# Optimization experiments

Hardware: AMD Instinct MI355X
Metric: run time of the kernel (lower is better)

The kernel has to match this reference:

```python
import jax, jax.numpy as jnp
import numpy as np

N = 262144
LOC_ENC_LEN = 60
NUM_WEIGHTS = 8
INDIM = 32
OUTDIM = 32
HIDDEN = 32
NEG_SLOPE = 0.01  # nn.LeakyReLU default


def _linear_init(key, fan_in, fan_out):
    # torch nn.Linear default: U(-1/sqrt(fan_in), 1/sqrt(fan_in))
    kw, kb = jax.random.split(key)
    bound = 1.0 / np.sqrt(fan_in)
    w = jax.random.uniform(kw, (fan_in, fan_out), jnp.float32, -bound, bound)
    b = jax.random.uniform(kb, (fan_out,), jnp.float32, -bound, bound)
    return w, b


def setup_inputs() -> dict:
    key = jax.random.key(0)
    ks = jax.random.split(key, 10)
    rel_loc_feat = jax.random.normal(ks[0], (N, LOC_ENC_LEN), jnp.float32)
    feat = jax.random.normal(ks[1], (N, INDIM), jnp.float32)
    dims = [LOC_ENC_LEN, HIDDEN, HIDDEN, HIDDEN, HIDDEN, HIDDEN, NUM_WEIGHTS]
    params = {}
    for i in range(6):
        w, b = _linear_init(ks[2 + i], dims[i], dims[i + 1])
        params[f'sn_w{i}'] = w
        params[f'sn_b{i}'] = b
    # weights_bank: kaiming_normal on [num_weights, indim*outdim] -> std = sqrt(2/fan_in), fan_in = indim*outdim
    std = np.sqrt(2.0 / (INDIM * OUTDIM))
    params['bank'] = jax.random.normal(ks[9], (NUM_WEIGHTS, INDIM * OUTDIM), jnp.float32) * std
    return {'rel_loc_feat': rel_loc_feat, 'feat': feat, **params}


def _score_net(x, ws, bs):
    # 5 Linear+LeakyReLU blocks, then final Linear (no activation)
    for i in range(5):
        x = x @ ws[i] + bs[i]
        x = jnp.where(x >= 0, x, NEG_SLOPE * x)
    return x @ ws[5] + bs[5]


def reference(rel_loc_feat, feat,
              sn_w0, sn_b0, sn_w1, sn_b1, sn_w2, sn_b2,
              sn_w3, sn_b3, sn_w4, sn_b4, sn_w5, sn_b5, bank):
    ws = [sn_w0, sn_w1, sn_w2, sn_w3, sn_w4, sn_w5]
    bs = [sn_b0, sn_b1, sn_b2, sn_b3, sn_b4, sn_b5]
    logits = _score_net(rel_loc_feat, ws, bs)          # [N, num_weights]
    coeff = jax.nn.softmax(logits, axis=-1)            # [N, num_weights]
    # per-point weight matrix: [N, indim*outdim] -> [N, indim, outdim]
    weights = (coeff @ bank).reshape(coeff.shape[0], INDIM, OUTDIM)
    # per-point matmul: feat[:, None] @ weights -> squeeze
    out = jnp.einsum('ni,nio->no', feat, weights)      # [N, outdim]
    return out
```

## Files before the change

### kernel.cpp

```cpp
#include <hip/hip_runtime.h>
#include <stdint.h>


typedef __attribute__((ext_vector_type(8))) __bf16 bf16x8;
typedef __attribute__((ext_vector_type(4))) float f32x4;

union FragU { uint32_t u[4]; bf16x8 v; uint4 q; };

__device__ __forceinline__ unsigned short f2bf(float f) {
    union { float f; uint32_t i; } v; v.f = f;
    return (unsigned short)((v.i + 0x7FFFu + ((v.i >> 16) & 1u)) >> 16);
}
__device__ __forceinline__ float bf2f(uint32_t u16) {
    union { uint32_t i; float f; } v; v.i = u16 << 16; return v.f;
}
__device__ __forceinline__ uint32_t pk2(float x, float y) {
    return (uint32_t)f2bf(x) | ((uint32_t)f2bf(y) << 16);
}
__device__ __forceinline__ int permK(int k) {
    return 4 * (k >> 3) + (k & 3) + 16 * ((k >> 2) & 1);
}
__device__ __forceinline__ f32x4 MF(bf16x8 a, bf16x8 b, f32x4 c) {
    return __builtin_amdgcn_mfma_f32_16x16x32_bf16(a, b, c, 0, 0, 0);
}


struct WPf { const float* p[13]; };

__global__ void pc_prep(WPf wp, uint32_t* __restrict__ ws) {
    int idx = blockIdx.x * blockDim.x + threadIdx.x;
    if (idx >= 10240) return;
    if (idx < 7424) {
        int layer, t, chunk = 0, lane, d; const float* w; bool perm;
        int r = idx;
        if (r < 1024) { chunk = r >> 9; r &= 511; t = r >> 8; r &= 255; lane = r >> 2; d = r & 3;
                        layer = 0; w = wp.p[0]; perm = false; }
        else if (r < 3072) { r -= 1024; layer = 1 + (r >> 9); r &= 511; t = r >> 8; r &= 255;
                             lane = r >> 2; d = r & 3; w = wp.p[2 * layer]; perm = true; }
        else if (r < 3328) { r -= 3072; layer = 5; t = 0; lane = r >> 2; d = r & 3;
                             w = wp.p[10]; perm = true; }
        else { r -= 3328; int bk = r >> 9; r &= 511; t = r >> 8; r &= 255; lane = r >> 2; d = r & 3;
               layer = -1; w = wp.p[12] + bk * 1024; perm = false; }
        int gq = lane >> 4, m = t * 16 + (lane & 15);
        uint32_t o = 0;
        #pragma unroll
        for (int e = 0; e < 2; ++e) {
            int kf = 8 * gq + 2 * d + e;
            float v = 0.f;
            if (layer == -1) {
                v = w[kf * 32 + m];
            } else {
                int ks = perm ? permK(kf) : (chunk * 32 + kf);
                if (layer == 0)      { if (ks < 60) v = w[ks * 32 + m]; }
                else if (layer == 5) { if (m < 8)   v = w[ks * 8 + m]; }
                else                 v = w[ks * 32 + m];
            }
            o |= ((uint32_t)f2bf(v)) << (16 * e);
        }
        ws[idx] = o;
    } else if (idx < 9984) {
        int r = idx - 7424; int L = r >> 9; r &= 511; int t = r >> 8; r &= 255;
        int lane = r >> 2, rr = r & 3;
        ((float*)ws)[idx] = wp.p[2 * L + 1][t * 16 + 4 * (lane >> 4) + rr];
    } else {
        int r = idx - 9984; int lane = r >> 2, rr = r & 3;
        int m = 4 * (lane >> 4) + rr;
        ((float*)ws)[idx] = (m < 8) ? wp.p[11][m] : 0.f;
    }
}

#define IT 2

__global__ __launch_bounds__(256, 4) void pc_main(
    const float* __restrict__ rel, const float* __restrict__ feat,
    const uint32_t* __restrict__ wsu, float* __restrict__ out)
{
    __shared__ __align__(16) uint32_t W[7424];
    {
        uint4* s4 = (uint4*)W;
        const uint4* g4 = (const uint4*)wsu;
        for (int i = threadIdx.x; i < 1856; i += 256) s4[i] = g4[i];
    }
    __syncthreads();

    const int lane = threadIdx.x & 63;
    const int wv = threadIdx.x >> 6;
    const int g = lane >> 4;
    const int n16 = lane & 15;

    const float* bw = (const float*)wsu;
    f32x4 Bi[5][2], Bi5;
    #pragma unroll
    for (int L = 0; L < 5; ++L)
        #pragma unroll
        for (int t = 0; t < 2; ++t) {
            float4 b = ((const float4*)(bw + 7424 + L * 512 + t * 256))[lane];
            Bi[L][t][0] = b.x; Bi[L][t][1] = b.y; Bi[L][t][2] = b.z; Bi[L][t][3] = b.w;
        }
    {
        float4 b = ((const float4*)(bw + 9984))[lane];
        Bi5[0] = b.x; Bi5[1] = b.y; Bi5[2] = b.z; Bi5[3] = b.w;
    }

    const size_t pt0 = (size_t)(blockIdx.x * 4 + wv) * (16 * IT);

    #define LDF(off) ({ FragU _f; _f.q = ((const uint4*)(W + (off)))[lane]; _f.v; })

    #pragma unroll
    for (int it = 0; it < IT; ++it) {
        const size_t n = pt0 + (size_t)it * 16 + n16;

        const float* rrow = rel + n * 60;
        float4 ra = *(const float4*)(rrow + 8 * g);
        float4 rb = *(const float4*)(rrow + 8 * g + 4);
        float4 rc = *(const float4*)(rrow + 32 + 8 * g);
        float4 rd = make_float4(0.f, 0.f, 0.f, 0.f);
        if (g < 3) rd = *(const float4*)(rrow + 36 + 8 * g);
        const float* frow = feat + n * 32 + 8 * g;
        float4 fa = *(const float4*)frow;
        float4 fb = *(const float4*)(frow + 4);

        FragU b0, b1;
        b0.u[0] = pk2(ra.x, ra.y); b0.u[1] = pk2(ra.z, ra.w);
        b0.u[2] = pk2(rb.x, rb.y); b0.u[3] = pk2(rb.z, rb.w);
        b1.u[0] = pk2(rc.x, rc.y); b1.u[1] = pk2(rc.z, rc.w);
        b1.u[2] = pk2(rd.x, rd.y); b1.u[3] = pk2(rd.z, rd.w);

        f32x4 t0 = Bi[0][0], t1 = Bi[0][1];
        t0 = MF(LDF(0),   b0.v, t0); t1 = MF(LDF(256), b0.v, t1);
        t0 = MF(LDF(512), b1.v, t0); t1 = MF(LDF(768), b1.v, t1);

        #pragma unroll
        for (int L = 0; L < 4; ++L) {
            FragU bx;
            #pragma unroll
            for (int r = 0; r < 4; ++r) {
                t0[r] = fmaxf(t0[r], 0.01f * t0[r]);
                t1[r] = fmaxf(t1[r], 0.01f * t1[r]);
            }
            bx.u[0] = pk2(t0[0], t0[1]); bx.u[1] = pk2(t0[2], t0[3]);
            bx.u[2] = pk2(t1[0], t1[1]); bx.u[3] = pk2(t1[2], t1[3]);
            t0 = MF(LDF(1024 + L * 512),       bx.v, Bi[L + 1][0]);
            t1 = MF(LDF(1024 + L * 512 + 256), bx.v, Bi[L + 1][1]);
        }

        {
            FragU bx;
            #pragma unroll
            for (int r = 0; r < 4; ++r) {
                t0[r] = fmaxf(t0[r], 0.01f * t0[r]);
                t1[r] = fmaxf(t1[r], 0.01f * t1[r]);
            }
            bx.u[0] = pk2(t0[0], t0[1]); bx.u[1] = pk2(t0[2], t0[3]);
            bx.u[2] = pk2(t1[0], t1[1]); bx.u[3] = pk2(t1[2], t1[3]);
            t0 = MF(LDF(3072), bx.v, Bi5);
        }

        float m4 = fmaxf(fmaxf(t0[0], t0[1]), fmaxf(t0[2], t0[3]));
        float m8 = fmaxf(m4, __shfl_xor(m4, 16, 64));
        float e0 = __expf(t0[0] - m8), e1 = __expf(t0[1] - m8);
        float e2 = __expf(t0[2] - m8), e3 = __expf(t0[3] - m8);
        float s4 = e0 + e1 + e2 + e3;
        float s8 = s4 + __shfl_xor(s4, 16, 64);
        float inv = 1.0f / s8;
        uint32_t p01 = pk2(e0 * inv, e1 * inv);
        uint32_t p23 = pk2(e2 * inv, e3 * inv);
        uint32_t q01 = (uint32_t)__builtin_amdgcn_ds_bpermute(n16 * 4, (int)p01);
        uint32_t q23 = (uint32_t)__builtin_amdgcn_ds_bpermute(n16 * 4, (int)p23);
        uint32_t q45 = (uint32_t)__builtin_amdgcn_ds_bpermute((n16 + 16) * 4, (int)p01);
        uint32_t q67 = (uint32_t)__builtin_amdgcn_ds_bpermute((n16 + 16) * 4, (int)p23);
        float cw[8] = { bf2f(q01 & 0xffff), bf2f(q01 >> 16),
                        bf2f(q23 & 0xffff), bf2f(q23 >> 16),
                        bf2f(q45 & 0xffff), bf2f(q45 >> 16),
                        bf2f(q67 & 0xffff), bf2f(q67 >> 16) };

        FragU bf_;
        bf_.u[0] = pk2(fa.x, fa.y); bf_.u[1] = pk2(fa.z, fa.w);
        bf_.u[2] = pk2(fb.x, fb.y); bf_.u[3] = pk2(fb.z, fb.w);

        f32x4 o0 = {0.f, 0.f, 0.f, 0.f}, o1 = {0.f, 0.f, 0.f, 0.f};
        #pragma unroll
        for (int k = 0; k < 8; ++k) {
            f32x4 z = {0.f, 0.f, 0.f, 0.f};
            f32x4 u0 = MF(LDF(3328 + k * 512),       bf_.v, z);
            f32x4 u1 = MF(LDF(3328 + k * 512 + 256), bf_.v, z);
            #pragma unroll
            for (int r = 0; r < 4; ++r) {
                o0[r] += cw[k] * u0[r];
                o1[r] += cw[k] * u1[r];
            }
        }

        float* orow = out + n * 32;
        *(float4*)(orow + 4 * g)      = make_float4(o0[0], o0[1], o0[2], o0[3]);
        *(float4*)(orow + 16 + 4 * g) = make_float4(o1[0], o1[1], o1[2], o1[3]);
    }
    #undef LDF
}

extern "C" void kernel_launch(void* const* d_in, const int* in_sizes, int n_in,
                              void* d_out, int out_size, void* d_ws, size_t ws_size,
                              hipStream_t stream)
{
    const float* rel = (const float*)d_in[0];
    const float* feat = (const float*)d_in[1];
    WPf wp;
    for (int i = 0; i < 13; ++i) wp.p[i] = (const float*)d_in[2 + i];
    uint32_t* ws = (uint32_t*)d_ws;
    float* out = (float*)d_out;

    const int npts = in_sizes[0] / 60;
    const int nblocks = npts / (16 * IT * 4);

    hipLaunchKernelGGL(pc_prep, dim3(40), dim3(256), 0, stream, wp, ws);
    hipLaunchKernelGGL(pc_main, dim3(nblocks), dim3(256), 0, stream, rel, feat, ws, out);
}
```

Before: 163.1 us.

## Hold score-net weight fragments in registers, shrink LDS, cheaper bf16 packing

The score-net A fragments (layers 0-5) now load from global memory into registers once per wave, and only the 8 bank fragments stay in LDS (16KB instead of about 29KB). The per-block LDS fill and the per-iteration LDS reads for the MLP go away. Each wave now handles 4 point tiles (IT 4, unroll 2) with launch bounds lowered to 3 blocks/CU to make room for the extra registers. bf16 packing switches to round-half-up plus v_perm, which saves ALU work but changes rounding slightly (no longer round-to-nearest-even).

```diff
diff --git a/kernel.cpp b/kernel.cpp
--- a/kernel.cpp
+++ b/kernel.cpp
@@ -14,8 +14,9 @@
 __device__ __forceinline__ float bf2f(uint32_t u16) {
     union { uint32_t i; float f; } v; v.i = u16 << 16; return v.f;
 }
-__device__ __forceinline__ uint32_t pk2(float x, float y) {
-    return (uint32_t)f2bf(x) | ((uint32_t)f2bf(y) << 16);
+__device__ __forceinline__ uint32_t pk2f(float x, float y) {
+    union { float f; uint32_t i; } a, b; a.f = x; b.f = y;
+    return __builtin_amdgcn_perm(b.i + 0x8000u, a.i + 0x8000u, 0x07060302u);
 }
 __device__ __forceinline__ int permK(int k) {
     return 4 * (k >> 3) + (k & 3) + 16 * ((k >> 2) & 1);
@@ -69,17 +70,18 @@
     }
 }
 
-#define IT 2
-
-__global__ __launch_bounds__(256, 4) void pc_main(
+#define IT 4
+
+__global__ __launch_bounds__(256, 3) void pc_main(
     const float* __restrict__ rel, const float* __restrict__ feat,
     const uint32_t* __restrict__ wsu, float* __restrict__ out)
 {
-    __shared__ __align__(16) uint32_t W[7424];
+    __shared__ __align__(16) uint32_t WB[4096];
     {
-        uint4* s4 = (uint4*)W;
-        const uint4* g4 = (const uint4*)wsu;
-        for (int i = threadIdx.x; i < 1856; i += 256) s4[i] = g4[i];
+        uint4* s4 = (uint4*)WB;
+        const uint4* g4 = (const uint4*)wsu + 832;
+        #pragma unroll
+        for (int i = 0; i < 4; ++i) s4[threadIdx.x + 256 * i] = g4[threadIdx.x + 256 * i];
     }
     __syncthreads();
 
@@ -88,6 +90,18 @@
     const int g = lane >> 4;
     const int n16 = lane & 15;
 
+    #define LDG(off) ({ FragU _f; _f.q = ((const uint4*)(wsu + (off)))[lane]; _f.v; })
+    const bf16x8 A00 = LDG(0),   A01 = LDG(256);
+    const bf16x8 A10 = LDG(512), A11 = LDG(768);
+    bf16x8 A14[4][2];
+    #pragma unroll
+    for (int L = 0; L < 4; ++L) {
+        A14[L][0] = LDG(1024 + L * 512);
+        A14[L][1] = LDG(1024 + L * 512 + 256);
+    }
+    const bf16x8 A5 = LDG(3072);
+    #undef LDG
+
     const float* bw = (const float*)wsu;
     f32x4 Bi[5][2], Bi5;
     #pragma unroll
@@ -104,9 +118,9 @@
 
     const size_t pt0 = (size_t)(blockIdx.x * 4 + wv) * (16 * IT);
 
-    #define LDF(off) ({ FragU _f; _f.q = ((const uint4*)(W + (off)))[lane]; _f.v; })
-
-    #pragma unroll
+    #define LDS_F(off) ({ FragU _f; _f.q = ((const uint4*)(WB + (off)))[lane]; _f.v; })
+
+    #pragma unroll 2
     for (int it = 0; it < IT; ++it) {
         const size_t n = pt0 + (size_t)it * 16 + n16;
 
@@ -121,14 +135,14 @@
         float4 fb = *(const float4*)(frow + 4);
 
         FragU b0, b1;
-        b0.u[0] = pk2(ra.x, ra.y); b0.u[1] = pk2(ra.z, ra.w);
-        b0.u[2] = pk2(rb.x, rb.y); b0.u[3] = pk2(rb.z, rb.w);
-        b1.u[0] = pk2(rc.x, rc.y); b1.u[1] = pk2(rc.z, rc.w);
-        b1.u[2] = pk2(rd.x, rd.y); b1.u[3] = pk2(rd.z, rd.w);
+        b0.u[0] = pk2f(ra.x, ra.y); b0.u[1] = pk2f(ra.z, ra.w);
+        b0.u[2] = pk2f(rb.x, rb.y); b0.u[3] = pk2f(rb.z, rb.w);
+        b1.u[0] = pk2f(rc.x, rc.y); b1.u[1] = pk2f(rc.z, rc.w);
+        b1.u[2] = pk2f(rd.x, rd.y); b1.u[3] = pk2f(rd.z, rd.w);
 
         f32x4 t0 = Bi[0][0], t1 = Bi[0][1];
-        t0 = MF(LDF(0),   b0.v, t0); t1 = MF(LDF(256), b0.v, t1);
-        t0 = MF(LDF(512), b1.v, t0); t1 = MF(LDF(768), b1.v, t1);
+        t0 = MF(A00, b0.v, t0); t1 = MF(A01, b0.v, t1);
+        t0 = MF(A10, b1.v, t0); t1 = MF(A11, b1.v, t1);
 
         #pragma unroll
         for (int L = 0; L < 4; ++L) {
@@ -138,10 +152,10 @@
                 t0[r] = fmaxf(t0[r], 0.01f * t0[r]);
                 t1[r] = fmaxf(t1[r], 0.01f * t1[r]);
             }
-            bx.u[0] = pk2(t0[0], t0[1]); bx.u[1] = pk2(t0[2], t0[3]);
-            bx.u[2] = pk2(t1[0], t1[1]); bx.u[3] = pk2(t1[2], t1[3]);
-            t0 = MF(LDF(1024 + L * 512),       bx.v, Bi[L + 1][0]);
-            t1 = MF(LDF(1024 + L * 512 + 256), bx.v, Bi[L + 1][1]);
+            bx.u[0] = pk2f(t0[0], t0[1]); bx.u[1] = pk2f(t0[2], t0[3]);
+            bx.u[2] = pk2f(t1[0], t1[1]); bx.u[3] = pk2f(t1[2], t1[3]);
+            t0 = MF(A14[L][0], bx.v, Bi[L + 1][0]);
+            t1 = MF(A14[L][1], bx.v, Bi[L + 1][1]);
         }
 
         {
@@ -151,9 +165,9 @@
                 t0[r] = fmaxf(t0[r], 0.01f * t0[r]);
                 t1[r] = fmaxf(t1[r], 0.01f * t1[r]);
             }
-            bx.u[0] = pk2(t0[0], t0[1]); bx.u[1] = pk2(t0[2], t0[3]);
-            bx.u[2] = pk2(t1[0], t1[1]); bx.u[3] = pk2(t1[2], t1[3]);
-            t0 = MF(LDF(3072), bx.v, Bi5);
+            bx.u[0] = pk2f(t0[0], t0[1]); bx.u[1] = pk2f(t0[2], t0[3]);
+            bx.u[2] = pk2f(t1[0], t1[1]); bx.u[3] = pk2f(t1[2], t1[3]);
+            t0 = MF(A5, bx.v, Bi5);
         }
 
         float m4 = fmaxf(fmaxf(t0[0], t0[1]), fmaxf(t0[2], t0[3]));
@@ -163,8 +177,8 @@
         float s4 = e0 + e1 + e2 + e3;
         float s8 = s4 + __shfl_xor(s4, 16, 64);
         float inv = 1.0f / s8;
-        uint32_t p01 = pk2(e0 * inv, e1 * inv);
-        uint32_t p23 = pk2(e2 * inv, e3 * inv);
+        uint32_t p01 = pk2f(e0 * inv, e1 * inv);
+        uint32_t p23 = pk2f(e2 * inv, e3 * inv);
         uint32_t q01 = (uint32_t)__builtin_amdgcn_ds_bpermute(n16 * 4, (int)p01);
         uint32_t q23 = (uint32_t)__builtin_amdgcn_ds_bpermute(n16 * 4, (int)p23);
         uint32_t q45 = (uint32_t)__builtin_amdgcn_ds_bpermute((n16 + 16) * 4, (int)p01);
@@ -175,15 +189,15 @@
                         bf2f(q67 & 0xffff), bf2f(q67 >> 16) };
 
         FragU bf_;
-        bf_.u[0] = pk2(fa.x, fa.y); bf_.u[1] = pk2(fa.z, fa.w);
-        bf_.u[2] = pk2(fb.x, fb.y); bf_.u[3] = pk2(fb.z, fb.w);
+        bf_.u[0] = pk2f(fa.x, fa.y); bf_.u[1] = pk2f(fa.z, fa.w);
+        bf_.u[2] = pk2f(fb.x, fb.y); bf_.u[3] = pk2f(fb.z, fb.w);
 
         f32x4 o0 = {0.f, 0.f, 0.f, 0.f}, o1 = {0.f, 0.f, 0.f, 0.f};
         #pragma unroll
         for (int k = 0; k < 8; ++k) {
             f32x4 z = {0.f, 0.f, 0.f, 0.f};
-            f32x4 u0 = MF(LDF(3328 + k * 512),       bf_.v, z);
-            f32x4 u1 = MF(LDF(3328 + k * 512 + 256), bf_.v, z);
+            f32x4 u0 = MF(LDS_F(k * 512),       bf_.v, z);
+            f32x4 u1 = MF(LDS_F(k * 512 + 256), bf_.v, z);
             #pragma unroll
             for (int r = 0; r < 4; ++r) {
                 o0[r] += cw[k] * u0[r];
@@ -195,7 +209,7 @@
         *(float4*)(orow + 4 * g)      = make_float4(o0[0], o0[1], o0[2], o0[3]);
         *(float4*)(orow + 16 + 4 * g) = make_float4(o1[0], o1[1], o1[2], o1[3]);
     }
-    #undef LDF
+    #undef LDS_F
 }
 
 extern "C" void kernel_launch(void* const* d_in, const int* in_sizes, int n_in,
```

After: 223.2 us. 1.37x slower.
